# Performance work log

Hardware: AMD Instinct MI355X
Metric: run time of the kernel (lower is better)

The kernel has to match this reference:

```python
import jax, jax.numpy as jnp
import numpy as np

D_IN = 64   # T (condition_length)
D = 128     # latent_dim
H = 8       # num_head
N = 2       # batch of graphs
M = 512     # num_nodes
T_OBS = 5.0


def leaky(v):
    return jnp.where(v >= 0, v, 0.2 * v)


def setup_inputs() -> dict:
    key = jax.random.key(0)
    ks = jax.random.split(key, 24)
    g = lambda k, s: jax.random.normal(k, s, dtype=jnp.float32) * 0.05
    return {
        "x": jax.random.normal(ks[0], (N, M, D_IN), dtype=jnp.float32),
        # f_node: T -> 2D -> D
        "fn_w1": g(ks[1], (D_IN, 2 * D)), "fn_b1": g(ks[2], (2 * D,)),
        "fn_w2": g(ks[3], (2 * D, D)),   "fn_b2": g(ks[4], (D,)),
        # per-head K/Q/V projections, stacked over heads
        "wk": g(ks[5], (H, D, D)), "bk": g(ks[6], (H, D)),
        "wq": g(ks[7], (H, D, D)), "bq": g(ks[8], (H, D)),
        "wv": g(ks[9], (H, D, D)), "bv": g(ks[10], (H, D)),
        # f_v: H*D -> D -> D
        "fv_w1": g(ks[11], (H * D, D)), "fv_b1": g(ks[12], (D,)),
        "fv_w2": g(ks[13], (D, D)),     "fv_b2": g(ks[14], (D,)),
        # f_node2edge: 2D -> D -> 1
        "fe_w1": g(ks[15], (2 * D, D)), "fe_b1": g(ks[16], (D,)),
        "fe_w2": g(ks[17], (D, 1)),     "fe_b2": g(ks[18], (1,)),
    }


def reference(x, fn_w1, fn_b1, fn_w2, fn_b2, wk, bk, wq, bq, wv, bv,
              fv_w1, fv_b1, fv_w2, fv_b2, fe_w1, fe_b1, fe_w2, fe_b2):
    n, m, T = x.shape
    # TemporalEncoding with d_hid=1: div_term = [1.0], even col -> sin(t)
    t = jnp.linspace(0.0, T_OBS, T)
    te = jnp.sin(t)  # [T]
    # f_node
    h = jax.nn.relu((x + te) @ fn_w1 + fn_b1) @ fn_w2 + fn_b2  # [N,M,D]
    # per-head attention (sender=K_i, receiver=Q_j -> scores = K Q^T)
    K = jnp.einsum('nmd,hde->hnme', h, wk) + bk[:, None, None, :]
    Q = jnp.einsum('nmd,hde->hnme', h, wq) + bq[:, None, None, :]
    V = jnp.einsum('nmd,hde->hnme', h, wv) + bv[:, None, None, :]
    scores = jnp.einsum('hnid,hnjd->hnij', K, Q)           # [H,N,M,M]
    alpha = jax.nn.softmax(leaky(scores), axis=-1)
    att = leaky(jnp.einsum('hnij,hnjd->hnid', alpha, V))   # [H,N,M,D]
    # concat heads along feature dim (head 0 first)
    att = jnp.transpose(att, (1, 2, 0, 3)).reshape(n, m, -1)  # [N,M,H*D]
    x2 = jax.nn.relu(att @ fv_w1 + fv_b1) @ fv_w2 + fv_b2 + h  # [N,M,D]
    # pairwise node2edge FFN: pair(i,j) = concat(x2_i, x2_j)
    half = fe_w1.shape[0] // 2
    A = x2 @ fe_w1[:half]   # contribution of node i
    B = x2 @ fe_w1[half:]   # contribution of node j
    hid = jax.nn.relu(A[:, :, None, :] + B[:, None, :, :] + fe_b1)  # [N,M,M,D]
    edge = (hid @ fe_w2 + fe_b2)[..., 0] / float(m)  # [N,M,M]
    return (x2, edge)
```

## Files before the change

kernel.cpp:

```cpp
#include <hip/hip_runtime.h>

typedef unsigned short u16;
typedef unsigned int u32;
typedef __attribute__((ext_vector_type(8))) short short8;
typedef __attribute__((ext_vector_type(4))) float f32x4;

__device__ __forceinline__ u16 f2b(float f) {
  union { float f; u32 i; } v; v.f = f;
  u32 i = v.i;
  return (u16)((i + 0x7FFFu + ((i >> 16) & 1u)) >> 16);
}
__device__ __forceinline__ float lo16(u32 x) { union { u32 i; float f; } v; v.i = x << 16; return v.f; }
__device__ __forceinline__ float hi16(u32 x) { union { u32 i; float f; } v; v.i = x & 0xffff0000u; return v.f; }
__device__ __forceinline__ u32 pack2(float a, float b) { return (u32)f2b(a) | ((u32)f2b(b) << 16); }

__device__ __align__(16) float g_h[1024 * 128];
__device__ __align__(16) u16   g_hb[1024 * 128];
__device__ __align__(16) u16   g_Wt[24 * 128 * 128];
__device__ __align__(16) u16   g_w1t[128 * 1024];
__device__ __align__(16) u16   g_w2t[128 * 128];
__device__ __align__(16) u16   g_fat[2 * 128 * 128];
__device__ __align__(16) u16   g_K[16 * 512 * 128];
__device__ __align__(16) u16   g_Q[16 * 512 * 128];
__device__ __align__(16) u16   g_V[16 * 512 * 128];
__device__ __align__(16) u16   g_Opb[512 * 64 * 128];
__device__ __align__(16) float g_ml[512 * 64 * 2];
__device__ __align__(16) float g_A[1024 * 128];
__device__ __align__(16) float g_Bm[1024 * 128];

__global__ void k_fnode(const float* __restrict__ x, const float* __restrict__ w1,
                        const float* __restrict__ b1, const float* __restrict__ w2,
                        const float* __restrict__ b2, const float* __restrict__ wk,
                        const float* __restrict__ wq, const float* __restrict__ wv,
                        const float* __restrict__ fvw1, const float* __restrict__ fvw2,
                        const float* __restrict__ few1) {
  __shared__ float xr[2 * 64];
  __shared__ float hids[2 * 256];
  __shared__ float red[2048];
  int tx = threadIdx.x;
  int row0 = blockIdx.x * 2;
  if (tx < 128) {
    int r = tx >> 6, k = tx & 63;
    xr[tx] = x[(row0 + r) * 64 + k] + sinf((float)k * (5.0f / 63.0f));
  }
  {
    int base = blockIdx.x * 1280 + tx;
#pragma unroll
    for (int t = 0; t < 5; t++) {
      int idx = base + t * 256;
      if (idx < 393216) {
        int ph = idx >> 14, rem = idx & 16383, e = rem >> 7, d = rem & 127;
        int proj = ph >> 3, head = ph & 7;
        const float* W = (proj == 0) ? wk : (proj == 1) ? wq : wv;
        g_Wt[idx] = f2b(W[head * 16384 + d * 128 + e]);
      } else if (idx < 524288) {
        int idx2 = idx - 393216;
        int e = idx2 >> 10, k = idx2 & 1023;
        g_w1t[idx2] = f2b(fvw1[k * 128 + e]);
      } else if (idx < 540672) {
        int idx3 = idx - 524288;
        int e = idx3 >> 7, k = idx3 & 127;
        g_w2t[idx3] = f2b(fvw2[k * 128 + e]);
      } else if (idx < 573440) {
        int idx4 = idx - 540672;
        int half = idx4 >> 14, rem = idx4 & 16383;
        int e = rem >> 7, k = rem & 127;
        g_fat[idx4] = f2b(few1[(half * 128 + k) * 128 + e]);
      }
    }
  }
  __syncthreads();
  {
    int ks = tx >> 6, cg = tx & 63;
    float acc[2][4] = {};
#pragma unroll 4
    for (int i = 0; i < 16; i++) {
      int k = ks * 16 + i;
      float4 w4 = *(const float4*)&w1[k * 256 + cg * 4];
      float a0 = xr[k], a1 = xr[64 + k];
      acc[0][0] = fmaf(a0, w4.x, acc[0][0]); acc[0][1] = fmaf(a0, w4.y, acc[0][1]);
      acc[0][2] = fmaf(a0, w4.z, acc[0][2]); acc[0][3] = fmaf(a0, w4.w, acc[0][3]);
      acc[1][0] = fmaf(a1, w4.x, acc[1][0]); acc[1][1] = fmaf(a1, w4.y, acc[1][1]);
      acc[1][2] = fmaf(a1, w4.z, acc[1][2]); acc[1][3] = fmaf(a1, w4.w, acc[1][3]);
    }
#pragma unroll
    for (int r = 0; r < 2; r++)
      *(float4*)&red[ks * 512 + r * 256 + cg * 4] = *(float4*)acc[r];
  }
  __syncthreads();
#pragma unroll
  for (int jo = 0; jo < 2; jo++) {
    int o = jo * 256 + tx;
    float s = red[o] + red[512 + o] + red[1024 + o] + red[1536 + o];
    hids[o] = fmaxf(s + b1[o & 255], 0.0f);
  }
  __syncthreads();
  {
    int ks = tx >> 5, eg = tx & 31;
    float acc[2][4] = {};
#pragma unroll 4
    for (int i = 0; i < 32; i++) {
      int k = ks * 32 + i;
      float4 w4 = *(const float4*)&w2[k * 128 + eg * 4];
      float a0 = hids[k], a1 = hids[256 + k];
      acc[0][0] = fmaf(a0, w4.x, acc[0][0]); acc[0][1] = fmaf(a0, w4.y, acc[0][1]);
      acc[0][2] = fmaf(a0, w4.z, acc[0][2]); acc[0][3] = fmaf(a0, w4.w, acc[0][3]);
      acc[1][0] = fmaf(a1, w4.x, acc[1][0]); acc[1][1] = fmaf(a1, w4.y, acc[1][1]);
      acc[1][2] = fmaf(a1, w4.z, acc[1][2]); acc[1][3] = fmaf(a1, w4.w, acc[1][3]);
    }
    __syncthreads();
#pragma unroll
    for (int r = 0; r < 2; r++)
      *(float4*)&red[ks * 256 + r * 128 + eg * 4] = *(float4*)acc[r];
  }
  __syncthreads();
  {
    float s = 0.0f;
#pragma unroll
    for (int ks = 0; ks < 8; ks++) s += red[ks * 256 + tx];
    int r = tx >> 7, e = tx & 127;
    float v = s + b2[e];
    g_h[(row0 + r) * 128 + e] = v;
    g_hb[(row0 + r) * 128 + e] = f2b(v);
  }
}

__global__ __launch_bounds__(256) void k_kqv(
    const float* __restrict__ bk, const float* __restrict__ bq,
    const float* __restrict__ bv) {
  __shared__ u16 hs[64 * 136];
  __shared__ u16 Wt[128 * 136];
  int b = blockIdx.x, tx = threadIdx.x;
  int rt = b & 15, ph = b >> 4;
  int proj = ph >> 3, head = ph & 7;
  const float* Bb = (proj == 0) ? bk : (proj == 1) ? bq : bv;
  u16* O = (proj == 0) ? g_K : (proj == 1) ? g_Q : g_V;
  int r0 = rt * 64;
#pragma unroll
  for (int t = 0; t < 4; t++) {
    int idx = t * 256 + tx, row = idx >> 4, oct = idx & 15;
    *(uint4*)&hs[row * 136 + oct * 8] = *(const uint4*)&g_hb[(r0 + row) * 128 + oct * 8];
  }
  const u16* Wtg = g_Wt + ph * 16384;
#pragma unroll
  for (int t = 0; t < 8; t++) {
    int idx = t * 256 + tx, row = idx >> 4, oct = idx & 15;
    *(uint4*)&Wt[row * 136 + oct * 8] = *(const uint4*)&Wtg[row * 128 + oct * 8];
  }
  __syncthreads();
  int lane = tx & 63, wv_ = tx >> 6, cl = lane & 15, quad = lane >> 4;
  short8 bH[4];
#pragma unroll
  for (int kk = 0; kk < 4; kk++)
    bH[kk] = *(const short8*)&hs[(wv_ * 16 + cl) * 136 + kk * 32 + quad * 8];
  f32x4 zero = {0.0f, 0.0f, 0.0f, 0.0f};
  f32x4 acc[8];
#pragma unroll
  for (int em = 0; em < 8; em++) acc[em] = zero;
#pragma unroll
  for (int em = 0; em < 8; em++)
#pragma unroll
    for (int kk = 0; kk < 4; kk++) {
      short8 aW = *(const short8*)&Wt[(em * 16 + cl) * 136 + kk * 32 + quad * 8];
      acc[em] = __builtin_amdgcn_mfma_f32_16x16x32_bf16(aW, bH[kk], acc[em], 0, 0, 0);
    }
#pragma unroll
  for (int em = 0; em < 8; em++) {
    float4 b4 = *(const float4*)&Bb[head * 128 + em * 16 + quad * 4];
    uint2 st = make_uint2(pack2(acc[em][0] + b4.x, acc[em][1] + b4.y),
                          pack2(acc[em][2] + b4.z, acc[em][3] + b4.w));
    *(uint2*)&O[(head * 1024 + r0 + wv_ * 16 + cl) * 128 + em * 16 + quad * 4] = st;
  }
}

__global__ __launch_bounds__(256) void k_attn() {
  __shared__ u16 Ks[64 * 136];
  __shared__ u16 Qs[64 * 136];
  __shared__ u16 Vt[128 * 72];
  __shared__ u16 Pw[4 * 16 * 72];
  __shared__ float alphas[4 * 16];
  int b = blockIdx.x, tx = threadIdx.x;
  int jc = b & 3, it = (b >> 2) & 7, hn = b >> 5;
  int i0 = it * 64;
  const u16* Kp = g_K + hn * 65536;
  const u16* Qp = g_Q + hn * 65536;
  const u16* Vp = g_V + hn * 65536;
#pragma unroll
  for (int t = 0; t < 4; t++) {
    int idx = t * 256 + tx, row = idx >> 4, oct = idx & 15;
    *(uint4*)&Ks[row * 136 + oct * 8] = *(const uint4*)&Kp[(i0 + row) * 128 + oct * 8];
  }
  int lane = tx & 63, wv = tx >> 6;
  int cl = lane & 15, quad = lane >> 4;
  f32x4 zero = {0.0f, 0.0f, 0.0f, 0.0f};
  f32x4 o[8];
#pragma unroll
  for (int es = 0; es < 8; es++) o[es] = zero;
  float m_ = -1e30f, l_ = 0.0f;

  for (int jt = 0; jt < 2; jt++) {
    int j0 = jc * 128 + jt * 64;
    __syncthreads();
#pragma unroll
    for (int t = 0; t < 4; t++) {
      int idx = t * 256 + tx, row = idx >> 4, oct = idx & 15;
      *(uint4*)&Qs[row * 136 + oct * 8] = *(const uint4*)&Qp[(j0 + row) * 128 + oct * 8];
    }
    {
      int jg = (tx & 15) * 4, e8 = (tx >> 4) * 8;
      uint4 r0 = *(const uint4*)&Vp[(j0 + jg + 0) * 128 + e8];
      uint4 r1 = *(const uint4*)&Vp[(j0 + jg + 1) * 128 + e8];
      uint4 r2 = *(const uint4*)&Vp[(j0 + jg + 2) * 128 + e8];
      uint4 r3 = *(const uint4*)&Vp[(j0 + jg + 3) * 128 + e8];
      const u32* p0 = (const u32*)&r0; const u32* p1 = (const u32*)&r1;
      const u32* p2 = (const u32*)&r2; const u32* p3 = (const u32*)&r3;
#pragma unroll
      for (int c = 0; c < 8; c++) {
        int w = c >> 1, sh = (c & 1) * 16;
        u32 lo = ((p0[w] >> sh) & 0xffffu) | (((p1[w] >> sh) & 0xffffu) << 16);
        u32 hi = ((p2[w] >> sh) & 0xffffu) | (((p3[w] >> sh) & 0xffffu) << 16);
        *(uint2*)&Vt[(e8 + c) * 72 + jg] = make_uint2(lo, hi);
      }
    }
    __syncthreads();
    short8 bK[4];
#pragma unroll
    for (int kk = 0; kk < 4; kk++)
      bK[kk] = *(const short8*)&Ks[(wv * 16 + cl) * 136 + kk * 32 + quad * 8];
    f32x4 st[4];
#pragma unroll
    for (int s = 0; s < 4; s++) {
      f32x4 acc = zero;
#pragma unroll
      for (int kk = 0; kk < 4; kk++) {
        short8 aQ = *(const short8*)&Qs[(s * 16 + cl) * 136 + kk * 32 + quad * 8];
        acc = __builtin_amdgcn_mfma_f32_16x16x32_bf16(aQ, bK[kk], acc, 0, 0, 0);
      }
      st[s] = acc;
    }
    float p[4][4];
    float tm = -1e30f;
#pragma unroll
    for (int s = 0; s < 4; s++)
#pragma unroll
      for (int r = 0; r < 4; r++) {
        float v = st[s][r];
        v = fmaxf(v, 0.2f * v);
        p[s][r] = v;
        tm = fmaxf(tm, v);
      }
    tm = fmaxf(tm, __shfl_xor(tm, 16));
    tm = fmaxf(tm, __shfl_xor(tm, 32));
    float mn = fmaxf(m_, tm);
    float alpha = __expf(m_ - mn);
    m_ = mn;
    float ps = 0.0f;
#pragma unroll
    for (int s = 0; s < 4; s++)
#pragma unroll
      for (int r = 0; r < 4; r++) {
        float e = __expf(p[s][r] - mn);
        p[s][r] = e;
        ps += e;
      }
    ps += __shfl_xor(ps, 16);
    ps += __shfl_xor(ps, 32);
    l_ = l_ * alpha + ps;
#pragma unroll
    for (int s = 0; s < 4; s++) {
      uint2 w2v = make_uint2(pack2(p[s][0], p[s][1]), pack2(p[s][2], p[s][3]));
      *(uint2*)&Pw[(wv * 16 + cl) * 72 + s * 16 + quad * 4] = w2v;
    }
    if (quad == 0) alphas[wv * 16 + cl] = alpha;
    __syncthreads();
    f32x4 av = *(const f32x4*)&alphas[wv * 16 + quad * 4];
#pragma unroll
    for (int es = 0; es < 8; es++) o[es] *= av;
    short8 aP[2];
#pragma unroll
    for (int k2 = 0; k2 < 2; k2++)
      aP[k2] = *(const short8*)&Pw[(wv * 16 + cl) * 72 + k2 * 32 + quad * 8];
#pragma unroll
    for (int es = 0; es < 8; es++) {
#pragma unroll
      for (int k2 = 0; k2 < 2; k2++) {
        short8 bV = *(const short8*)&Vt[(es * 16 + cl) * 72 + k2 * 32 + quad * 8];
        o[es] = __builtin_amdgcn_mfma_f32_16x16x32_bf16(aP[k2], bV, o[es], 0, 0, 0);
      }
    }
  }
#pragma unroll
  for (int es = 0; es < 8; es++)
#pragma unroll
    for (int r = 0; r < 4; r++)
      g_Opb[(b * 64 + wv * 16 + quad * 4 + r) * 128 + es * 16 + cl] = f2b(o[es][r]);
  if (quad == 0) {
    g_ml[(b * 64 + wv * 16 + cl) * 2 + 0] = m_;
    g_ml[(b * 64 + wv * 16 + cl) * 2 + 1] = l_;
  }
}

__global__ __launch_bounds__(256) void k_fv(
    const float* __restrict__ fv_b1, const float* __restrict__ fv_b2,
    const float* __restrict__ fe_b1, float* __restrict__ x2out) {
  __shared__ u16 atts[16 * 1032];
  __shared__ u16 wst[128 * 136];
  __shared__ u16 hidb[16 * 136];
  __shared__ u16 x2b[16 * 136];
  int b = blockIdx.x, tx = threadIdx.x;
  int r0 = b * 16;

  {
    int task = tx >> 1, half = tx & 1;
    int lr = task >> 3, head = task & 7;
    int gr = r0 + lr;
    int n = gr >> 9, i = gr & 511;
    int it = i >> 6, lr64 = i & 63;
    int hn = head * 2 + n;
    int mlbase = (hn * 32 + it * 4) * 64 + lr64;
    float mc[4], lc[4];
#pragma unroll
    for (int c = 0; c < 4; c++) {
      float2 ml = *(const float2*)&g_ml[(mlbase + c * 64) * 2];
      mc[c] = ml.x; lc[c] = ml.y;
    }
    float ms = fmaxf(fmaxf(mc[0], mc[1]), fmaxf(mc[2], mc[3]));
    float lsum = 0.0f;
    float ra[64];
#pragma unroll
    for (int i2 = 0; i2 < 64; i2++) ra[i2] = 0.0f;
#pragma unroll
    for (int c = 0; c < 4; c++) {
      float w = __expf(mc[c] - ms);
      lsum += w * lc[c];
      const u16* src = &g_Opb[(mlbase + c * 64) * 128 + half * 64];
#pragma unroll
      for (int ov = 0; ov < 8; ov++) {
        uint4 v = *(const uint4*)&src[ov * 8];
        ra[ov * 8 + 0] = fmaf(w, lo16(v.x), ra[ov * 8 + 0]);
        ra[ov * 8 + 1] = fmaf(w, hi16(v.x), ra[ov * 8 + 1]);
        ra[ov * 8 + 2] = fmaf(w, lo16(v.y), ra[ov * 8 + 2]);
        ra[ov * 8 + 3] = fmaf(w, hi16(v.y), ra[ov * 8 + 3]);
        ra[ov * 8 + 4] = fmaf(w, lo16(v.z), ra[ov * 8 + 4]);
        ra[ov * 8 + 5] = fmaf(w, hi16(v.z), ra[ov * 8 + 5]);
        ra[ov * 8 + 6] = fmaf(w, lo16(v.w), ra[ov * 8 + 6]);
        ra[ov * 8 + 7] = fmaf(w, hi16(v.w), ra[ov * 8 + 7]);
      }
    }
    float inv = 1.0f / lsum;
    u32 pk[32];
#pragma unroll
    for (int i2 = 0; i2 < 32; i2++) {
      float v0 = ra[i2 * 2] * inv;     v0 = fmaxf(v0, 0.2f * v0);
      float v1 = ra[i2 * 2 + 1] * inv; v1 = fmaxf(v1, 0.2f * v1);
      pk[i2] = pack2(v0, v1);
    }
    int dst = lr * 1032 + head * 128 + half * 64;
#pragma unroll
    for (int ov = 0; ov < 8; ov++)
      *(uint4*)&atts[dst + ov * 8] =
          make_uint4(pk[ov * 4], pk[ov * 4 + 1], pk[ov * 4 + 2], pk[ov * 4 + 3]);
  }
  __syncthreads();

  int lane = tx & 63, w = tx >> 6, cl = lane & 15, quad = lane >> 4;
  f32x4 zero = {0.0f, 0.0f, 0.0f, 0.0f};

  f32x4 accH[2] = {zero, zero};
  for (int kc = 0; kc < 8; kc++) {
#pragma unroll
    for (int q = 0; q < 8; q++) {
      int idx = q * 256 + tx, row = idx >> 4, oct = idx & 15;
      *(uint4*)&wst[row * 136 + oct * 8] =
          *(const uint4*)&g_w1t[row * 1024 + kc * 128 + oct * 8];
    }
    __syncthreads();
    short8 bA[4];
#pragma unroll
    for (int kk = 0; kk < 4; kk++)
      bA[kk] = *(const short8*)&atts[cl * 1032 + kc * 128 + kk * 32 + quad * 8];
#pragma unroll
    for (int t2 = 0; t2 < 2; t2++) {
      int em = 2 * w + t2;
#pragma unroll
      for (int kk = 0; kk < 4; kk++) {
        short8 aW = *(const short8*)&wst[(em * 16 + cl) * 136 + kk * 32 + quad * 8];
        accH[t2] = __builtin_amdgcn_mfma_f32_16x16x32_bf16(aW, bA[kk], accH[t2], 0, 0, 0);
      }
    }
    __syncthreads();
  }

#pragma unroll
  for (int t2 = 0; t2 < 2; t2++) {
    int eb = (2 * w + t2) * 16 + quad * 4;
    float4 b4 = *(const float4*)&fv_b1[eb];
    float v0 = fmaxf(accH[t2][0] + b4.x, 0.0f);
    float v1 = fmaxf(accH[t2][1] + b4.y, 0.0f);
    float v2 = fmaxf(accH[t2][2] + b4.z, 0.0f);
    float v3 = fmaxf(accH[t2][3] + b4.w, 0.0f);
    *(u32*)&hidb[cl * 136 + eb] = pack2(v0, v1);
    *(u32*)&hidb[cl * 136 + eb + 2] = pack2(v2, v3);
  }
#pragma unroll
  for (int q = 0; q < 8; q++) {
    int idx = q * 256 + tx, row = idx >> 4, oct = idx & 15;
    *(uint4*)&wst[row * 136 + oct * 8] = *(const uint4*)&g_w2t[row * 128 + oct * 8];
  }
  __syncthreads();

  {
    short8 bH2[4];
#pragma unroll
    for (int kk = 0; kk < 4; kk++)
      bH2[kk] = *(const short8*)&hidb[cl * 136 + kk * 32 + quad * 8];
    int gr = r0 + cl;
#pragma unroll
    for (int t2 = 0; t2 < 2; t2++) {
      int em = 2 * w + t2;
      f32x4 acc2 = zero;
#pragma unroll
      for (int kk = 0; kk < 4; kk++) {
        short8 aW = *(const short8*)&wst[(em * 16 + cl) * 136 + kk * 32 + quad * 8];
        acc2 = __builtin_amdgcn_mfma_f32_16x16x32_bf16(aW, bH2[kk], acc2, 0, 0, 0);
      }
      int eb = em * 16 + quad * 4;
      float4 b4 = *(const float4*)&fv_b2[eb];
      float4 h4 = *(const float4*)&g_h[gr * 128 + eb];
      float4 xv;
      xv.x = acc2[0] + b4.x + h4.x;
      xv.y = acc2[1] + b4.y + h4.y;
      xv.z = acc2[2] + b4.z + h4.z;
      xv.w = acc2[3] + b4.w + h4.w;
      *(float4*)&x2out[gr * 128 + eb] = xv;
      *(u32*)&x2b[cl * 136 + eb] = pack2(xv.x, xv.y);
      *(u32*)&x2b[cl * 136 + eb + 2] = pack2(xv.z, xv.w);
    }
  }
  __syncthreads();

#pragma unroll
  for (int q = 0; q < 8; q++) {
    int idx = q * 256 + tx, row = idx >> 4, oct = idx & 15;
    *(uint4*)&wst[row * 136 + oct * 8] = *(const uint4*)&g_fat[row * 128 + oct * 8];
  }
  __syncthreads();
  short8 bX[4];
#pragma unroll
  for (int kk = 0; kk < 4; kk++)
    bX[kk] = *(const short8*)&x2b[cl * 136 + kk * 32 + quad * 8];
  {
    int gr = r0 + cl;
#pragma unroll
    for (int t2 = 0; t2 < 2; t2++) {
      int em = 2 * w + t2;
      f32x4 accA = zero;
#pragma unroll
      for (int kk = 0; kk < 4; kk++) {
        short8 aW = *(const short8*)&wst[(em * 16 + cl) * 136 + kk * 32 + quad * 8];
        accA = __builtin_amdgcn_mfma_f32_16x16x32_bf16(aW, bX[kk], accA, 0, 0, 0);
      }
      int eb = em * 16 + quad * 4;
      float4 b4 = *(const float4*)&fe_b1[eb];
      float4 av;
      av.x = accA[0] + b4.x; av.y = accA[1] + b4.y;
      av.z = accA[2] + b4.z; av.w = accA[3] + b4.w;
      *(float4*)&g_A[gr * 128 + eb] = av;
    }
  }
  __syncthreads();

#pragma unroll
  for (int q = 0; q < 8; q++) {
    int idx = q * 256 + tx, row = idx >> 4, oct = idx & 15;
    *(uint4*)&wst[row * 136 + oct * 8] =
        *(const uint4*)&g_fat[16384 + row * 128 + oct * 8];
  }
  __syncthreads();
  {
    int gr = r0 + cl;
#pragma unroll
    for (int t2 = 0; t2 < 2; t2++) {
      int em = 2 * w + t2;
      f32x4 accB = zero;
#pragma unroll
      for (int kk = 0; kk < 4; kk++) {
        short8 aW = *(const short8*)&wst[(em * 16 + cl) * 136 + kk * 32 + quad * 8];
        accB = __builtin_amdgcn_mfma_f32_16x16x32_bf16(aW, bX[kk], accB, 0, 0, 0);
      }
      int eb = em * 16 + quad * 4;
      *(f32x4*)&g_Bm[gr * 128 + eb] = accB;
    }
  }
}

__global__ void k_edge(const float* __restrict__ few2, const float* __restrict__ feb2,
                       float* __restrict__ edge) {
  __shared__ float As[4 * 128];
  __shared__ float w2s[128];
  int b = blockIdx.x, tx = threadIdx.x;
  int n = b >> 8, rest = b & 255, ig = rest >> 1, jh = rest & 1;
  int i0 = ig * 4;
  if (tx < 128) w2s[tx] = few2[tx];
  As[tx] = g_A[(n * 512 + i0) * 128 + tx];
  As[tx + 256] = g_A[(n * 512 + i0) * 128 + tx + 256];
  float eb2 = feb2[0];
  __syncthreads();
  int j = jh * 256 + tx;
  const float* B0 = &g_Bm[(n * 512 + j) * 128];
  float acc[4] = {};
#pragma unroll 4
  for (int dc = 0; dc < 32; dc++) {
    float4 bv = *(const float4*)&B0[dc * 4];
    float4 w4 = *(const float4*)&w2s[dc * 4];
#pragma unroll
    for (int i = 0; i < 4; i++) {
      float4 a4 = *(const float4*)&As[i * 128 + dc * 4];
      acc[i] = fmaf(fmaxf(a4.x + bv.x, 0.0f), w4.x, acc[i]);
      acc[i] = fmaf(fmaxf(a4.y + bv.y, 0.0f), w4.y, acc[i]);
      acc[i] = fmaf(fmaxf(a4.z + bv.z, 0.0f), w4.z, acc[i]);
      acc[i] = fmaf(fmaxf(a4.w + bv.w, 0.0f), w4.w, acc[i]);
    }
  }
  const float scale = 1.0f / 512.0f;
#pragma unroll
  for (int i = 0; i < 4; i++)
    edge[(n * 512 + i0 + i) * 512 + j] = (acc[i] + eb2) * scale;
}

extern "C" void kernel_launch(void* const* d_in, const int* in_sizes, int n_in,
                              void* d_out, int out_size, void* d_ws, size_t ws_size,
                              hipStream_t stream) {
  (void)in_sizes; (void)n_in; (void)out_size; (void)d_ws; (void)ws_size;
  const float* x     = (const float*)d_in[0];
  const float* fn_w1 = (const float*)d_in[1];
  const float* fn_b1 = (const float*)d_in[2];
  const float* fn_w2 = (const float*)d_in[3];
  const float* fn_b2 = (const float*)d_in[4];
  const float* wk    = (const float*)d_in[5];
  const float* bk    = (const float*)d_in[6];
  const float* wq    = (const float*)d_in[7];
  const float* bq    = (const float*)d_in[8];
  const float* wv    = (const float*)d_in[9];
  const float* bv    = (const float*)d_in[10];
  const float* fv_w1 = (const float*)d_in[11];
  const float* fv_b1 = (const float*)d_in[12];
  const float* fv_w2 = (const float*)d_in[13];
  const float* fv_b2 = (const float*)d_in[14];
  const float* fe_w1 = (const float*)d_in[15];
  const float* fe_b1 = (const float*)d_in[16];
  const float* fe_w2 = (const float*)d_in[17];
  const float* fe_b2 = (const float*)d_in[18];

  float* x2out = (float*)d_out;
  float* edge  = x2out + 131072;

  k_fnode<<<512, 256, 0, stream>>>(x, fn_w1, fn_b1, fn_w2, fn_b2, wk, wq, wv,
                                   fv_w1, fv_w2, fe_w1);
  k_kqv<<<384, 256, 0, stream>>>(bk, bq, bv);
  k_attn<<<512, 256, 0, stream>>>();
  k_fv<<<64, 256, 0, stream>>>(fv_b1, fv_b2, fe_b1, x2out);
  k_edge<<<512, 256, 0, stream>>>(fe_w2, fe_b2, edge);
}
```

Measured before the change: 144.1 us.

## Fuse five kernels into two persistent kernels with grid-wide atomic barriers

Merges fnode, kqv and attention into one kernel, and fv and edge into another. Stages inside each kernel are separated by a software grid barrier built from an atomic counter, which removes kernel launch gaps. k_fv also stops staging weights in shared memory and reads the bf16 weight fragments straight from global memory, which drops several syncthreads. The A and B projections are now computed in one loop. The barrier relies on all 512 blocks being resident at once (two per CU), and a wrong assumption there would deadlock or add spin overhead.

```diff
diff --git a/kernel.cpp b/kernel.cpp
--- a/kernel.cpp
+++ b/kernel.cpp
@@ -28,23 +28,47 @@
 __device__ __align__(16) float g_A[1024 * 128];
 __device__ __align__(16) float g_Bm[1024 * 128];
 
-__global__ void k_fnode(const float* __restrict__ x, const float* __restrict__ w1,
-                        const float* __restrict__ b1, const float* __restrict__ w2,
-                        const float* __restrict__ b2, const float* __restrict__ wk,
-                        const float* __restrict__ wq, const float* __restrict__ wv,
-                        const float* __restrict__ fvw1, const float* __restrict__ fvw2,
-                        const float* __restrict__ few1) {
-  __shared__ float xr[2 * 64];
-  __shared__ float hids[2 * 256];
-  __shared__ float red[2048];
-  int tx = threadIdx.x;
-  int row0 = blockIdx.x * 2;
+__device__ u32 g_c1, g_c2, g_c3;
+
+__device__ __forceinline__ void gbar(u32* ctr, u32& gen, bool have_gen) {
+  __syncthreads();
+  if (threadIdx.x == 0) {
+    __threadfence();
+    u32 t = __hip_atomic_fetch_add(ctr, 1u, __ATOMIC_RELAXED,
+                                   __HIP_MEMORY_SCOPE_AGENT);
+    if (!have_gen) gen = t >> 9;
+    u32 target = (gen + 1u) << 9;
+    while (__hip_atomic_load(ctr, __ATOMIC_RELAXED, __HIP_MEMORY_SCOPE_AGENT) <
+           target)
+      __builtin_amdgcn_s_sleep(8);
+  }
+  __syncthreads();
+  __threadfence();
+}
+
+struct SM1 { float xr[128]; float hids[512]; float red[2048]; };
+struct SM2 { u16 hs[64 * 136]; u16 Wt[128 * 136]; };
+struct SM3 { u16 Ks[64 * 136]; u16 Qs[64 * 136]; u16 Vt[128 * 72];
+             u16 Pw[4 * 16 * 72]; float alphas[64]; };
+struct SMfv { u16 atts[16 * 1032]; u16 hidb[16 * 136]; u16 x2b[16 * 136]; };
+struct SM6 { float As[512]; float w2s[128]; };
+union __align__(16) SMA { SM1 p1; SM2 p2; SM3 p3; };
+union __align__(16) SMB { SMfv pf; SM6 p6; };
+
+__device__ __forceinline__ void phase_fnode(SM1& sm, int b, int tx,
+    const float* __restrict__ x, const float* __restrict__ w1,
+    const float* __restrict__ b1, const float* __restrict__ w2,
+    const float* __restrict__ b2, const float* __restrict__ wk,
+    const float* __restrict__ wq, const float* __restrict__ wv,
+    const float* __restrict__ fvw1, const float* __restrict__ fvw2,
+    const float* __restrict__ few1) {
+  int row0 = b * 2;
   if (tx < 128) {
     int r = tx >> 6, k = tx & 63;
-    xr[tx] = x[(row0 + r) * 64 + k] + sinf((float)k * (5.0f / 63.0f));
-  }
-  {
-    int base = blockIdx.x * 1280 + tx;
+    sm.xr[tx] = x[(row0 + r) * 64 + k] + sinf((float)k * (5.0f / 63.0f));
+  }
+  {
+    int base = b * 1280 + tx;
 #pragma unroll
     for (int t = 0; t < 5; t++) {
       int idx = base + t * 256;
@@ -77,7 +101,7 @@
     for (int i = 0; i < 16; i++) {
       int k = ks * 16 + i;
       float4 w4 = *(const float4*)&w1[k * 256 + cg * 4];
-      float a0 = xr[k], a1 = xr[64 + k];
+      float a0 = sm.xr[k], a1 = sm.xr[64 + k];
       acc[0][0] = fmaf(a0, w4.x, acc[0][0]); acc[0][1] = fmaf(a0, w4.y, acc[0][1]);
       acc[0][2] = fmaf(a0, w4.z, acc[0][2]); acc[0][3] = fmaf(a0, w4.w, acc[0][3]);
       acc[1][0] = fmaf(a1, w4.x, acc[1][0]); acc[1][1] = fmaf(a1, w4.y, acc[1][1]);
@@ -85,14 +109,14 @@
     }
 #pragma unroll
     for (int r = 0; r < 2; r++)
-      *(float4*)&red[ks * 512 + r * 256 + cg * 4] = *(float4*)acc[r];
+      *(float4*)&sm.red[ks * 512 + r * 256 + cg * 4] = *(float4*)acc[r];
   }
   __syncthreads();
 #pragma unroll
   for (int jo = 0; jo < 2; jo++) {
     int o = jo * 256 + tx;
-    float s = red[o] + red[512 + o] + red[1024 + o] + red[1536 + o];
-    hids[o] = fmaxf(s + b1[o & 255], 0.0f);
+    float s = sm.red[o] + sm.red[512 + o] + sm.red[1024 + o] + sm.red[1536 + o];
+    sm.hids[o] = fmaxf(s + b1[o & 255], 0.0f);
   }
   __syncthreads();
   {
@@ -102,7 +126,7 @@
     for (int i = 0; i < 32; i++) {
       int k = ks * 32 + i;
       float4 w4 = *(const float4*)&w2[k * 128 + eg * 4];
-      float a0 = hids[k], a1 = hids[256 + k];
+      float a0 = sm.hids[k], a1 = sm.hids[256 + k];
       acc[0][0] = fmaf(a0, w4.x, acc[0][0]); acc[0][1] = fmaf(a0, w4.y, acc[0][1]);
       acc[0][2] = fmaf(a0, w4.z, acc[0][2]); acc[0][3] = fmaf(a0, w4.w, acc[0][3]);
       acc[1][0] = fmaf(a1, w4.x, acc[1][0]); acc[1][1] = fmaf(a1, w4.y, acc[1][1]);
@@ -111,13 +135,13 @@
     __syncthreads();
 #pragma unroll
     for (int r = 0; r < 2; r++)
-      *(float4*)&red[ks * 256 + r * 128 + eg * 4] = *(float4*)acc[r];
+      *(float4*)&sm.red[ks * 256 + r * 128 + eg * 4] = *(float4*)acc[r];
   }
   __syncthreads();
   {
     float s = 0.0f;
 #pragma unroll
-    for (int ks = 0; ks < 8; ks++) s += red[ks * 256 + tx];
+    for (int ks = 0; ks < 8; ks++) s += sm.red[ks * 256 + tx];
     int r = tx >> 7, e = tx & 127;
     float v = s + b2[e];
     g_h[(row0 + r) * 128 + e] = v;
@@ -125,12 +149,9 @@
   }
 }
 
-__global__ __launch_bounds__(256) void k_kqv(
+__device__ __forceinline__ void phase_kqv(SM2& sm, int b, int tx,
     const float* __restrict__ bk, const float* __restrict__ bq,
     const float* __restrict__ bv) {
-  __shared__ u16 hs[64 * 136];
-  __shared__ u16 Wt[128 * 136];
-  int b = blockIdx.x, tx = threadIdx.x;
   int rt = b & 15, ph = b >> 4;
   int proj = ph >> 3, head = ph & 7;
   const float* Bb = (proj == 0) ? bk : (proj == 1) ? bq : bv;
@@ -139,20 +160,20 @@
 #pragma unroll
   for (int t = 0; t < 4; t++) {
     int idx = t * 256 + tx, row = idx >> 4, oct = idx & 15;
-    *(uint4*)&hs[row * 136 + oct * 8] = *(const uint4*)&g_hb[(r0 + row) * 128 + oct * 8];
+    *(uint4*)&sm.hs[row * 136 + oct * 8] = *(const uint4*)&g_hb[(r0 + row) * 128 + oct * 8];
   }
   const u16* Wtg = g_Wt + ph * 16384;
 #pragma unroll
   for (int t = 0; t < 8; t++) {
     int idx = t * 256 + tx, row = idx >> 4, oct = idx & 15;
-    *(uint4*)&Wt[row * 136 + oct * 8] = *(const uint4*)&Wtg[row * 128 + oct * 8];
+    *(uint4*)&sm.Wt[row * 136 + oct * 8] = *(const uint4*)&Wtg[row * 128 + oct * 8];
   }
   __syncthreads();
   int lane = tx & 63, wv_ = tx >> 6, cl = lane & 15, quad = lane >> 4;
   short8 bH[4];
 #pragma unroll
   for (int kk = 0; kk < 4; kk++)
-    bH[kk] = *(const short8*)&hs[(wv_ * 16 + cl) * 136 + kk * 32 + quad * 8];
+    bH[kk] = *(const short8*)&sm.hs[(wv_ * 16 + cl) * 136 + kk * 32 + quad * 8];
   f32x4 zero = {0.0f, 0.0f, 0.0f, 0.0f};
   f32x4 acc[8];
 #pragma unroll
@@ -161,7 +182,7 @@
   for (int em = 0; em < 8; em++)
 #pragma unroll
     for (int kk = 0; kk < 4; kk++) {
-      short8 aW = *(const short8*)&Wt[(em * 16 + cl) * 136 + kk * 32 + quad * 8];
+      short8 aW = *(const short8*)&sm.Wt[(em * 16 + cl) * 136 + kk * 32 + quad * 8];
       acc[em] = __builtin_amdgcn_mfma_f32_16x16x32_bf16(aW, bH[kk], acc[em], 0, 0, 0);
     }
 #pragma unroll
@@ -173,13 +194,7 @@
   }
 }
 
-__global__ __launch_bounds__(256) void k_attn() {
-  __shared__ u16 Ks[64 * 136];
-  __shared__ u16 Qs[64 * 136];
-  __shared__ u16 Vt[128 * 72];
-  __shared__ u16 Pw[4 * 16 * 72];
-  __shared__ float alphas[4 * 16];
-  int b = blockIdx.x, tx = threadIdx.x;
+__device__ __forceinline__ void phase_attn(SM3& sm, int b, int tx) {
   int jc = b & 3, it = (b >> 2) & 7, hn = b >> 5;
   int i0 = it * 64;
   const u16* Kp = g_K + hn * 65536;
@@ -188,7 +203,7 @@
 #pragma unroll
   for (int t = 0; t < 4; t++) {
     int idx = t * 256 + tx, row = idx >> 4, oct = idx & 15;
-    *(uint4*)&Ks[row * 136 + oct * 8] = *(const uint4*)&Kp[(i0 + row) * 128 + oct * 8];
+    *(uint4*)&sm.Ks[row * 136 + oct * 8] = *(const uint4*)&Kp[(i0 + row) * 128 + oct * 8];
   }
   int lane = tx & 63, wv = tx >> 6;
   int cl = lane & 15, quad = lane >> 4;
@@ -204,7 +219,7 @@
 #pragma unroll
     for (int t = 0; t < 4; t++) {
       int idx = t * 256 + tx, row = idx >> 4, oct = idx & 15;
-      *(uint4*)&Qs[row * 136 + oct * 8] = *(const uint4*)&Qp[(j0 + row) * 128 + oct * 8];
+      *(uint4*)&sm.Qs[row * 136 + oct * 8] = *(const uint4*)&Qp[(j0 + row) * 128 + oct * 8];
     }
     {
       int jg = (tx & 15) * 4, e8 = (tx >> 4) * 8;
@@ -219,21 +234,21 @@
         int w = c >> 1, sh = (c & 1) * 16;
         u32 lo = ((p0[w] >> sh) & 0xffffu) | (((p1[w] >> sh) & 0xffffu) << 16);
         u32 hi = ((p2[w] >> sh) & 0xffffu) | (((p3[w] >> sh) & 0xffffu) << 16);
-        *(uint2*)&Vt[(e8 + c) * 72 + jg] = make_uint2(lo, hi);
+        *(uint2*)&sm.Vt[(e8 + c) * 72 + jg] = make_uint2(lo, hi);
       }
     }
     __syncthreads();
     short8 bK[4];
 #pragma unroll
     for (int kk = 0; kk < 4; kk++)
-      bK[kk] = *(const short8*)&Ks[(wv * 16 + cl) * 136 + kk * 32 + quad * 8];
+      bK[kk] = *(const short8*)&sm.Ks[(wv * 16 + cl) * 136 + kk * 32 + quad * 8];
     f32x4 st[4];
 #pragma unroll
     for (int s = 0; s < 4; s++) {
       f32x4 acc = zero;
 #pragma unroll
       for (int kk = 0; kk < 4; kk++) {
-        short8 aQ = *(const short8*)&Qs[(s * 16 + cl) * 136 + kk * 32 + quad * 8];
+        short8 aQ = *(const short8*)&sm.Qs[(s * 16 + cl) * 136 + kk * 32 + quad * 8];
         acc = __builtin_amdgcn_mfma_f32_16x16x32_bf16(aQ, bK[kk], acc, 0, 0, 0);
       }
       st[s] = acc;
@@ -269,22 +284,22 @@
 #pragma unroll
     for (int s = 0; s < 4; s++) {
       uint2 w2v = make_uint2(pack2(p[s][0], p[s][1]), pack2(p[s][2], p[s][3]));
-      *(uint2*)&Pw[(wv * 16 + cl) * 72 + s * 16 + quad * 4] = w2v;
-    }
-    if (quad == 0) alphas[wv * 16 + cl] = alpha;
+      *(uint2*)&sm.Pw[(wv * 16 + cl) * 72 + s * 16 + quad * 4] = w2v;
+    }
+    if (quad == 0) sm.alphas[wv * 16 + cl] = alpha;
     __syncthreads();
-    f32x4 av = *(const f32x4*)&alphas[wv * 16 + quad * 4];
+    f32x4 av = *(const f32x4*)&sm.alphas[wv * 16 + quad * 4];
 #pragma unroll
     for (int es = 0; es < 8; es++) o[es] *= av;
     short8 aP[2];
 #pragma unroll
     for (int k2 = 0; k2 < 2; k2++)
-      aP[k2] = *(const short8*)&Pw[(wv * 16 + cl) * 72 + k2 * 32 + quad * 8];
+      aP[k2] = *(const short8*)&sm.Pw[(wv * 16 + cl) * 72 + k2 * 32 + quad * 8];
 #pragma unroll
     for (int es = 0; es < 8; es++) {
 #pragma unroll
       for (int k2 = 0; k2 < 2; k2++) {
-        short8 bV = *(const short8*)&Vt[(es * 16 + cl) * 72 + k2 * 32 + quad * 8];
+        short8 bV = *(const short8*)&sm.Vt[(es * 16 + cl) * 72 + k2 * 32 + quad * 8];
         o[es] = __builtin_amdgcn_mfma_f32_16x16x32_bf16(aP[k2], bV, o[es], 0, 0, 0);
       }
     }
@@ -300,16 +315,10 @@
   }
 }
 
-__global__ __launch_bounds__(256) void k_fv(
+__device__ __forceinline__ void phase_fv(SMfv& sm, int b, int tx,
     const float* __restrict__ fv_b1, const float* __restrict__ fv_b2,
     const float* __restrict__ fe_b1, float* __restrict__ x2out) {
-  __shared__ u16 atts[16 * 1032];
-  __shared__ u16 wst[128 * 136];
-  __shared__ u16 hidb[16 * 136];
-  __shared__ u16 x2b[16 * 136];
-  int b = blockIdx.x, tx = threadIdx.x;
   int r0 = b * 16;
-
   {
     int task = tx >> 1, half = tx & 1;
     int lr = task >> 3, head = task & 7;
@@ -358,39 +367,30 @@
     int dst = lr * 1032 + head * 128 + half * 64;
 #pragma unroll
     for (int ov = 0; ov < 8; ov++)
-      *(uint4*)&atts[dst + ov * 8] =
+      *(uint4*)&sm.atts[dst + ov * 8] =
           make_uint4(pk[ov * 4], pk[ov * 4 + 1], pk[ov * 4 + 2], pk[ov * 4 + 3]);
   }
   __syncthreads();
 
   int lane = tx & 63, w = tx >> 6, cl = lane & 15, quad = lane >> 4;
   f32x4 zero = {0.0f, 0.0f, 0.0f, 0.0f};
+  int e0 = (2 * w) * 16 + cl, e1 = (2 * w + 1) * 16 + cl;
 
   f32x4 accH[2] = {zero, zero};
+#pragma unroll 2
   for (int kc = 0; kc < 8; kc++) {
-#pragma unroll
-    for (int q = 0; q < 8; q++) {
-      int idx = q * 256 + tx, row = idx >> 4, oct = idx & 15;
-      *(uint4*)&wst[row * 136 + oct * 8] =
-          *(const uint4*)&g_w1t[row * 1024 + kc * 128 + oct * 8];
-    }
-    __syncthreads();
     short8 bA[4];
 #pragma unroll
     for (int kk = 0; kk < 4; kk++)
-      bA[kk] = *(const short8*)&atts[cl * 1032 + kc * 128 + kk * 32 + quad * 8];
-#pragma unroll
-    for (int t2 = 0; t2 < 2; t2++) {
-      int em = 2 * w + t2;
-#pragma unroll
-      for (int kk = 0; kk < 4; kk++) {
-        short8 aW = *(const short8*)&wst[(em * 16 + cl) * 136 + kk * 32 + quad * 8];
-        accH[t2] = __builtin_amdgcn_mfma_f32_16x16x32_bf16(aW, bA[kk], accH[t2], 0, 0, 0);
-      }
-    }
-    __syncthreads();
-  }
-
+      bA[kk] = *(const short8*)&sm.atts[cl * 1032 + kc * 128 + kk * 32 + quad * 8];
+#pragma unroll
+    for (int kk = 0; kk < 4; kk++) {
+      short8 aW0 = *(const short8*)&g_w1t[e0 * 1024 + kc * 128 + kk * 32 + quad * 8];
+      short8 aW1 = *(const short8*)&g_w1t[e1 * 1024 + kc * 128 + kk * 32 + quad * 8];
+      accH[0] = __builtin_amdgcn_mfma_f32_16x16x32_bf16(aW0, bA[kk], accH[0], 0, 0, 0);
+      accH[1] = __builtin_amdgcn_mfma_f32_16x16x32_bf16(aW1, bA[kk], accH[1], 0, 0, 0);
+    }
+  }
 #pragma unroll
   for (int t2 = 0; t2 < 2; t2++) {
     int eb = (2 * w + t2) * 16 + quad * 4;
@@ -399,29 +399,23 @@
     float v1 = fmaxf(accH[t2][1] + b4.y, 0.0f);
     float v2 = fmaxf(accH[t2][2] + b4.z, 0.0f);
     float v3 = fmaxf(accH[t2][3] + b4.w, 0.0f);
-    *(u32*)&hidb[cl * 136 + eb] = pack2(v0, v1);
-    *(u32*)&hidb[cl * 136 + eb + 2] = pack2(v2, v3);
-  }
-#pragma unroll
-  for (int q = 0; q < 8; q++) {
-    int idx = q * 256 + tx, row = idx >> 4, oct = idx & 15;
-    *(uint4*)&wst[row * 136 + oct * 8] = *(const uint4*)&g_w2t[row * 128 + oct * 8];
-  }
-  __syncthreads();
-
+    *(u32*)&sm.hidb[cl * 136 + eb] = pack2(v0, v1);
+    *(u32*)&sm.hidb[cl * 136 + eb + 2] = pack2(v2, v3);
+  }
+  __syncthreads();
   {
     short8 bH2[4];
 #pragma unroll
     for (int kk = 0; kk < 4; kk++)
-      bH2[kk] = *(const short8*)&hidb[cl * 136 + kk * 32 + quad * 8];
+      bH2[kk] = *(const short8*)&sm.hidb[cl * 136 + kk * 32 + quad * 8];
     int gr = r0 + cl;
 #pragma unroll
     for (int t2 = 0; t2 < 2; t2++) {
-      int em = 2 * w + t2;
+      int em = 2 * w + t2, er = em * 16 + cl;
       f32x4 acc2 = zero;
 #pragma unroll
       for (int kk = 0; kk < 4; kk++) {
-        short8 aW = *(const short8*)&wst[(em * 16 + cl) * 136 + kk * 32 + quad * 8];
+        short8 aW = *(const short8*)&g_w2t[er * 128 + kk * 32 + quad * 8];
         acc2 = __builtin_amdgcn_mfma_f32_16x16x32_bf16(aW, bH2[kk], acc2, 0, 0, 0);
       }
       int eb = em * 16 + quad * 4;
@@ -433,32 +427,27 @@
       xv.z = acc2[2] + b4.z + h4.z;
       xv.w = acc2[3] + b4.w + h4.w;
       *(float4*)&x2out[gr * 128 + eb] = xv;
-      *(u32*)&x2b[cl * 136 + eb] = pack2(xv.x, xv.y);
-      *(u32*)&x2b[cl * 136 + eb + 2] = pack2(xv.z, xv.w);
-    }
-  }
-  __syncthreads();
-
-#pragma unroll
-  for (int q = 0; q < 8; q++) {
-    int idx = q * 256 + tx, row = idx >> 4, oct = idx & 15;
-    *(uint4*)&wst[row * 136 + oct * 8] = *(const uint4*)&g_fat[row * 128 + oct * 8];
+      *(u32*)&sm.x2b[cl * 136 + eb] = pack2(xv.x, xv.y);
+      *(u32*)&sm.x2b[cl * 136 + eb + 2] = pack2(xv.z, xv.w);
+    }
   }
   __syncthreads();
   short8 bX[4];
 #pragma unroll
   for (int kk = 0; kk < 4; kk++)
-    bX[kk] = *(const short8*)&x2b[cl * 136 + kk * 32 + quad * 8];
+    bX[kk] = *(const short8*)&sm.x2b[cl * 136 + kk * 32 + quad * 8];
   {
     int gr = r0 + cl;
 #pragma unroll
     for (int t2 = 0; t2 < 2; t2++) {
-      int em = 2 * w + t2;
-      f32x4 accA = zero;
+      int em = 2 * w + t2, er = em * 16 + cl;
+      f32x4 accA = zero, accB = zero;
 #pragma unroll
       for (int kk = 0; kk < 4; kk++) {
-        short8 aW = *(const short8*)&wst[(em * 16 + cl) * 136 + kk * 32 + quad * 8];
-        accA = __builtin_amdgcn_mfma_f32_16x16x32_bf16(aW, bX[kk], accA, 0, 0, 0);
+        short8 aWA = *(const short8*)&g_fat[er * 128 + kk * 32 + quad * 8];
+        short8 aWB = *(const short8*)&g_fat[16384 + er * 128 + kk * 32 + quad * 8];
+        accA = __builtin_amdgcn_mfma_f32_16x16x32_bf16(aWA, bX[kk], accA, 0, 0, 0);
+        accB = __builtin_amdgcn_mfma_f32_16x16x32_bf16(aWB, bX[kk], accB, 0, 0, 0);
       }
       int eb = em * 16 + quad * 4;
       float4 b4 = *(const float4*)&fe_b1[eb];
@@ -466,44 +455,19 @@
       av.x = accA[0] + b4.x; av.y = accA[1] + b4.y;
       av.z = accA[2] + b4.z; av.w = accA[3] + b4.w;
       *(float4*)&g_A[gr * 128 + eb] = av;
-    }
-  }
-  __syncthreads();
-
-#pragma unroll
-  for (int q = 0; q < 8; q++) {
-    int idx = q * 256 + tx, row = idx >> 4, oct = idx & 15;
-    *(uint4*)&wst[row * 136 + oct * 8] =
-        *(const uint4*)&g_fat[16384 + row * 128 + oct * 8];
-  }
-  __syncthreads();
-  {
-    int gr = r0 + cl;
-#pragma unroll
-    for (int t2 = 0; t2 < 2; t2++) {
-      int em = 2 * w + t2;
-      f32x4 accB = zero;
-#pragma unroll
-      for (int kk = 0; kk < 4; kk++) {
-        short8 aW = *(const short8*)&wst[(em * 16 + cl) * 136 + kk * 32 + quad * 8];
-        accB = __builtin_amdgcn_mfma_f32_16x16x32_bf16(aW, bX[kk], accB, 0, 0, 0);
-      }
-      int eb = em * 16 + quad * 4;
       *(f32x4*)&g_Bm[gr * 128 + eb] = accB;
     }
   }
 }
 
-__global__ void k_edge(const float* __restrict__ few2, const float* __restrict__ feb2,
-                       float* __restrict__ edge) {
-  __shared__ float As[4 * 128];
-  __shared__ float w2s[128];
-  int b = blockIdx.x, tx = threadIdx.x;
+__device__ __forceinline__ void phase_edge(SM6& sm, int b, int tx,
+    const float* __restrict__ few2, const float* __restrict__ feb2,
+    float* __restrict__ edge) {
   int n = b >> 8, rest = b & 255, ig = rest >> 1, jh = rest & 1;
   int i0 = ig * 4;
-  if (tx < 128) w2s[tx] = few2[tx];
-  As[tx] = g_A[(n * 512 + i0) * 128 + tx];
-  As[tx + 256] = g_A[(n * 512 + i0) * 128 + tx + 256];
+  if (tx < 128) sm.w2s[tx] = few2[tx];
+  sm.As[tx] = g_A[(n * 512 + i0) * 128 + tx];
+  sm.As[tx + 256] = g_A[(n * 512 + i0) * 128 + tx + 256];
   float eb2 = feb2[0];
   __syncthreads();
   int j = jh * 256 + tx;
@@ -512,10 +476,10 @@
 #pragma unroll 4
   for (int dc = 0; dc < 32; dc++) {
     float4 bv = *(const float4*)&B0[dc * 4];
-    float4 w4 = *(const float4*)&w2s[dc * 4];
+    float4 w4 = *(const float4*)&sm.w2s[dc * 4];
 #pragma unroll
     for (int i = 0; i < 4; i++) {
-      float4 a4 = *(const float4*)&As[i * 128 + dc * 4];
+      float4 a4 = *(const float4*)&sm.As[i * 128 + dc * 4];
       acc[i] = fmaf(fmaxf(a4.x + bv.x, 0.0f), w4.x, acc[i]);
       acc[i] = fmaf(fmaxf(a4.y + bv.y, 0.0f), w4.y, acc[i]);
       acc[i] = fmaf(fmaxf(a4.z + bv.z, 0.0f), w4.z, acc[i]);
@@ -526,6 +490,38 @@
 #pragma unroll
   for (int i = 0; i < 4; i++)
     edge[(n * 512 + i0 + i) * 512 + j] = (acc[i] + eb2) * scale;
+}
+
+__global__ __launch_bounds__(256, 2) void k_front(
+    const float* __restrict__ x, const float* __restrict__ fn_w1,
+    const float* __restrict__ fn_b1, const float* __restrict__ fn_w2,
+    const float* __restrict__ fn_b2, const float* __restrict__ wk,
+    const float* __restrict__ bk, const float* __restrict__ wq,
+    const float* __restrict__ bq, const float* __restrict__ wv,
+    const float* __restrict__ bv, const float* __restrict__ fv_w1,
+    const float* __restrict__ fv_w2, const float* __restrict__ fe_w1) {
+  __shared__ SMA sm;
+  int b = blockIdx.x, tx = threadIdx.x;
+  u32 gen = 0;
+  phase_fnode(sm.p1, b, tx, x, fn_w1, fn_b1, fn_w2, fn_b2, wk, wq, wv,
+              fv_w1, fv_w2, fe_w1);
+  gbar(&g_c1, gen, false);
+  if (b < 384) phase_kqv(sm.p2, b, tx, bk, bq, bv);
+  gbar(&g_c2, gen, true);
+  phase_attn(sm.p3, b, tx);
+}
+
+__global__ __launch_bounds__(256, 2) void k_back(
+    const float* __restrict__ fv_b1, const float* __restrict__ fv_b2,
+    const float* __restrict__ fe_b1, const float* __restrict__ few2,
+    const float* __restrict__ feb2, float* __restrict__ x2out,
+    float* __restrict__ edge) {
+  __shared__ SMB sm;
+  int b = blockIdx.x, tx = threadIdx.x;
+  u32 gen = 0;
+  if (b < 64) phase_fv(sm.pf, b, tx, fv_b1, fv_b2, fe_b1, x2out);
+  gbar(&g_c3, gen, false);
+  phase_edge(sm.p6, b, tx, few2, feb2, edge);
 }
 
 extern "C" void kernel_launch(void* const* d_in, const int* in_sizes, int n_in,
@@ -555,10 +551,7 @@
   float* x2out = (float*)d_out;
   float* edge  = x2out + 131072;
 
-  k_fnode<<<512, 256, 0, stream>>>(x, fn_w1, fn_b1, fn_w2, fn_b2, wk, wq, wv,
-                                   fv_w1, fv_w2, fe_w1);
-  k_kqv<<<384, 256, 0, stream>>>(bk, bq, bv);
-  k_attn<<<512, 256, 0, stream>>>();
-  k_fv<<<64, 256, 0, stream>>>(fv_b1, fv_b2, fe_b1, x2out);
-  k_edge<<<512, 256, 0, stream>>>(fe_w2, fe_b2, edge);
-}
+  k_front<<<512, 256, 0, stream>>>(x, fn_w1, fn_b1, fn_w2, fn_b2, wk, bk, wq, bq,
+                                   wv, bv, fv_w1, fv_w2, fe_w1);
+  k_back<<<512, 256, 0, stream>>>(fv_b1, fv_b2, fe_b1, fe_w2, fe_b2, x2out, edge);
+}
```

New measurement: 353.0 us. 145% more time.
